# Performance work log

Hardware: AMD Instinct MI355X
Metric: run time of the kernel (lower is better)

## Reference

```python
import jax, jax.numpy as jnp
import numpy as np

N_NODES = 50000
N_EDGES = 800000
D_FEAT = 96
HIDDEN = 96
AVG_DEG = 16.0


def setup_inputs() -> dict:
    key = jax.random.key(0)
    k1, k2, k3, k4, k5 = jax.random.split(key, 5)
    x = jax.random.normal(k1, (N_NODES, D_FEAT), dtype=jnp.float32)
    row = jax.random.randint(k2, (N_EDGES,), 0, N_NODES)
    col = jax.random.randint(k3, (N_EDGES,), 0, N_NODES)
    edge_index = jnp.stack([row, col]).astype(jnp.int32)  # [2, E]
    # normalized adjacency values ~ 1/degree scale
    edge_weight = jax.random.uniform(k4, (N_EDGES,), dtype=jnp.float32) / AVG_DEG
    # init_w: small normal + identity (random=False path)
    W = 0.1 * jax.random.normal(k5, (D_FEAT, HIDDEN), dtype=jnp.float32) + jnp.eye(D_FEAT, HIDDEN, dtype=jnp.float32)
    b = jnp.zeros((HIDDEN,), dtype=jnp.float32)
    return {"x": x, "W": W, "b": b, "edge_index": edge_index, "edge_weight": edge_weight}


def reference(x, W, b, edge_index, edge_weight):
    # dense projection + bias
    h = x @ W + b  # [N, H]
    # sparse adj matmul: out[i] = sum_e w_e * h[col_e] for row_e == i
    row, col = edge_index[0], edge_index[1]
    msgs = edge_weight[:, None] * h[col]  # [E, H]
    pre_nonlinearity = jax.ops.segment_sum(msgs, row, num_segments=N_NODES)  # [N, H]
    # inference path: no dropout (training=None)
    output = jax.nn.elu(pre_nonlinearity)
    return (pre_nonlinearity, output)
```

## Files before the change

kernel.cpp:

```cpp
#include <hip/hip_runtime.h>


#define D 96
#define BSHIFT 5
#define BROWS 32
#define CAP 768
#define CPAD 16
#define EB_CHUNK 3200
#define NBKT_MAX 1600
#define GR 64
#define KP 104

typedef unsigned long long u64;
typedef unsigned short u16;
typedef unsigned int u32;

typedef __attribute__((ext_vector_type(8))) __bf16 bf8_t;
typedef __attribute__((ext_vector_type(8))) short s8_t;
typedef __attribute__((ext_vector_type(4))) float f4_t;

__device__ __forceinline__ u16 f2bf(float f) {
  const u32 u = __float_as_uint(f);
  return (u16)((u + 0x7FFFu + ((u >> 16) & 1u)) >> 16);
}
__device__ __forceinline__ float bf2f(u16 s) {
  return __uint_as_float(((u32)s) << 16);
}

__device__ __forceinline__ f4_t mfma16(s8_t a, s8_t b, f4_t c) {
  return __builtin_amdgcn_mfma_f32_16x16x32_bf16(
      __builtin_bit_cast(bf8_t, a), __builtin_bit_cast(bf8_t, b), c, 0, 0, 0);
}

union __align__(16) FusedSmem {
  struct { u16 hi[96 * KP]; u16 lo[96 * KP]; } w;
  struct { int cnt[NBKT_MAX]; int cur[NBKT_MAX]; int rbuf[EB_CHUNK]; } bz;
};

__global__ __launch_bounds__(256) void fused_gemm_bucketize(
    const float* __restrict__ x, const float* __restrict__ W,
    const float* __restrict__ bias, u16* __restrict__ h16, int n_nodes,
    const int* __restrict__ rows, const int* __restrict__ cols,
    const float* __restrict__ ew, int* __restrict__ bcur,
    u64* __restrict__ tmp, int n_edges, int nbkt, int bb) {
  __shared__ FusedSmem sm;
  const int tid = threadIdx.x;

  if ((int)blockIdx.x < bb) {
    for (int i = tid; i < NBKT_MAX; i += 256) sm.bz.cnt[i] = 0;
    __syncthreads();
    const int e0 = blockIdx.x * EB_CHUNK;
    const int e1 = min(e0 + EB_CHUNK, n_edges);
    for (int e = e0 + tid; e < e1; e += 256) {
      const int r = rows[e];
      sm.bz.rbuf[e - e0] = r;
      atomicAdd(&sm.bz.cnt[r >> BSHIFT], 1);
    }
    __syncthreads();
    for (int b = tid; b < nbkt; b += 256) {
      const int c = sm.bz.cnt[b];
      sm.bz.cur[b] = (c > 0) ? atomicAdd(&bcur[b * CPAD], c) : 0;
    }
    __syncthreads();
    for (int e = e0 + tid; e < e1; e += 256) {
      const int r = sm.bz.rbuf[e - e0];
      const int b = r >> BSHIFT;
      const u64 u = ((u64)__float_as_uint(ew[e]) << 32) |
                    ((u64)(r & (BROWS - 1)) << 20) | (u64)(unsigned)cols[e];
      const int pos = atomicAdd(&sm.bz.cur[b], 1);
      if (pos < CAP) tmp[(size_t)b * CAP + pos] = u;
    }
  } else {
    for (int e = tid; e < 96 * 96; e += 256) {
      const int k = e / 96;
      const int n = e - k * 96;
      const float w = W[e];
      const u16 hb = f2bf(w);
      sm.w.hi[n * KP + k] = hb;
      sm.w.lo[n * KP + k] = f2bf(w - bf2f(hb));
    }
    __syncthreads();

    const int wid = tid >> 6;
    const int lane = tid & 63;
    const int l15 = lane & 15;
    const int g = lane >> 4;
    const int row0 = ((int)blockIdx.x - bb) * GR + wid * 16;

    const int ra = min(row0 + l15, n_nodes - 1);
    const float* xr = x + (size_t)ra * D;
    s8_t ah[3], al[3];
#pragma unroll
    for (int kt = 0; kt < 3; ++kt) {
      const float4 v0 = *(const float4*)(xr + kt * 32 + 8 * g);
      const float4 v1 = *(const float4*)(xr + kt * 32 + 8 * g + 4);
      const float vv[8] = {v0.x, v0.y, v0.z, v0.w, v1.x, v1.y, v1.z, v1.w};
#pragma unroll
      for (int j = 0; j < 8; ++j) {
        const u16 hb = f2bf(vv[j]);
        ah[kt][j] = (short)hb;
        al[kt][j] = (short)f2bf(vv[j] - bf2f(hb));
      }
    }

    f4_t acc[6];
#pragma unroll
    for (int n = 0; n < 6; ++n) {
      const float bv = bias[n * 16 + l15];
      acc[n][0] = bv; acc[n][1] = bv; acc[n][2] = bv; acc[n][3] = bv;
    }

#pragma unroll
    for (int kt = 0; kt < 3; ++kt) {
#pragma unroll
      for (int n = 0; n < 6; ++n) {
        const int wo = (n * 16 + l15) * KP + kt * 32 + 8 * g;
        const s8_t bh = *(const s8_t*)&sm.w.hi[wo];
        const s8_t bl = *(const s8_t*)&sm.w.lo[wo];
        acc[n] = mfma16(ah[kt], bh, acc[n]);
        acc[n] = mfma16(al[kt], bh, acc[n]);
        acc[n] = mfma16(ah[kt], bl, acc[n]);
      }
    }

#pragma unroll
    for (int n = 0; n < 6; ++n) {
#pragma unroll
      for (int r = 0; r < 4; ++r) {
        const int row = row0 + 4 * g + r;
        if (row < n_nodes)
          h16[(size_t)row * D + n * 16 + l15] = f2bf(acc[n][r]);
      }
    }
  }
}

__global__ __launch_bounds__(256) void bucket_gather_kernel(
    const int* __restrict__ bcur, const u64* __restrict__ tmp,
    const u16* __restrict__ h16, float* __restrict__ pre,
    float* __restrict__ out, int n_nodes) {
  __shared__ u64 raw[CAP];
  __shared__ u64 se[CAP];
  __shared__ int cnt[BROWS];
  __shared__ int off[BROWS + 1];
  __shared__ int cur[BROWS];
  const int tid = threadIdx.x;
  const int b = blockIdx.x;
  if (tid < BROWS) cnt[tid] = 0;
  __syncthreads();

  const int base = b * CAP;
  int count = bcur[b * CPAD];
  if (count > CAP) count = CAP;

  for (int k = tid; k < count; k += 256) {
    const u64 u = tmp[base + k];
    raw[k] = u;
    atomicAdd(&cnt[(int)((u >> 20) & (BROWS - 1))], 1);
  }
  __syncthreads();

  if (tid < BROWS) off[tid + 1] = cnt[tid];
  if (tid == 0) off[0] = 0;
  __syncthreads();
  for (int d = 1; d <= BROWS; d <<= 1) {
    int v = 0;
    if (tid <= BROWS && tid >= d) v = off[tid - d];
    __syncthreads();
    if (tid <= BROWS) off[tid] += v;
    __syncthreads();
  }
  if (tid < BROWS) cur[tid] = off[tid];
  __syncthreads();

  for (int k = tid; k < count; k += 256) {
    const u64 u = raw[k];
    const int rl = (int)((u >> 20) & (BROWS - 1));
    se[atomicAdd(&cur[rl], 1)] = u;
  }
  __syncthreads();

  const int g = tid >> 5;
  const int lane = tid & 31;
  const int row0 = b * BROWS;
#pragma unroll
  for (int j = 0; j < 4; ++j) {
    const int r = g * 4 + j;
    const int row = row0 + r;
    const int s = off[r], e = off[r + 1];
    float a0 = 0.f, a1 = 0.f, a2 = 0.f;
    int k = s;
    for (; k + 3 < e; k += 4) {
      const u64 u0 = se[k], u1 = se[k + 1], u2 = se[k + 2], u3 = se[k + 3];
      const u16* h0 = h16 + (size_t)(u0 & 0xFFFFF) * D;
      const u16* h1 = h16 + (size_t)(u1 & 0xFFFFF) * D;
      const u16* h2 = h16 + (size_t)(u2 & 0xFFFFF) * D;
      const u16* h3 = h16 + (size_t)(u3 & 0xFFFFF) * D;
      const float w0 = __uint_as_float((u32)(u0 >> 32));
      const float w1 = __uint_as_float((u32)(u1 >> 32));
      const float w2 = __uint_as_float((u32)(u2 >> 32));
      const float w3 = __uint_as_float((u32)(u3 >> 32));
      const float p00 = bf2f(h0[lane]), p01 = bf2f(h0[lane + 32]), p02 = bf2f(h0[lane + 64]);
      const float p10 = bf2f(h1[lane]), p11 = bf2f(h1[lane + 32]), p12 = bf2f(h1[lane + 64]);
      const float p20 = bf2f(h2[lane]), p21 = bf2f(h2[lane + 32]), p22 = bf2f(h2[lane + 64]);
      const float p30 = bf2f(h3[lane]), p31 = bf2f(h3[lane + 32]), p32 = bf2f(h3[lane + 64]);
      a0 = fmaf(w0, p00, a0); a1 = fmaf(w0, p01, a1); a2 = fmaf(w0, p02, a2);
      a0 = fmaf(w1, p10, a0); a1 = fmaf(w1, p11, a1); a2 = fmaf(w1, p12, a2);
      a0 = fmaf(w2, p20, a0); a1 = fmaf(w2, p21, a1); a2 = fmaf(w2, p22, a2);
      a0 = fmaf(w3, p30, a0); a1 = fmaf(w3, p31, a1); a2 = fmaf(w3, p32, a2);
    }
    for (; k < e; ++k) {
      const u64 u = se[k];
      const u16* hr = h16 + (size_t)(u & 0xFFFFF) * D;
      const float w = __uint_as_float((u32)(u >> 32));
      a0 = fmaf(w, bf2f(hr[lane]), a0);
      a1 = fmaf(w, bf2f(hr[lane + 32]), a1);
      a2 = fmaf(w, bf2f(hr[lane + 64]), a2);
    }
    if (row < n_nodes) {
      float* pr = pre + (size_t)row * D;
      float* orow = out + (size_t)row * D;
      pr[lane] = a0; pr[lane + 32] = a1; pr[lane + 64] = a2;
      orow[lane]      = a0 > 0.f ? a0 : (__expf(a0) - 1.f);
      orow[lane + 32] = a1 > 0.f ? a1 : (__expf(a1) - 1.f);
      orow[lane + 64] = a2 > 0.f ? a2 : (__expf(a2) - 1.f);
    }
  }
}

extern "C" void kernel_launch(void* const* d_in, const int* in_sizes, int n_in,
                              void* d_out, int out_size, void* d_ws, size_t ws_size,
                              hipStream_t stream) {
  const float* x  = (const float*)d_in[0];
  const float* W  = (const float*)d_in[1];
  const float* b  = (const float*)d_in[2];
  const int*   ei = (const int*)d_in[3];
  const float* ew = (const float*)d_in[4];

  const int n_nodes = in_sizes[0] / D;
  const int n_edges = in_sizes[4];
  const int* rows = ei;
  const int* cols = ei + n_edges;

  float* pre  = (float*)d_out;
  float* outp = pre + (size_t)n_nodes * D;

  const int nbkt = (n_nodes + BROWS - 1) / BROWS;

  char* ws = (char*)d_ws;
  u16*  h16  = (u16*)ws;   ws += (size_t)n_nodes * D * sizeof(u16);
  int*  bcur = (int*)ws;   ws += (size_t)nbkt * CPAD * sizeof(int);
  u64*  tmp  = (u64*)ws;

  hipMemsetAsync(bcur, 0, (size_t)nbkt * CPAD * sizeof(int), stream);

  const int gb = (n_nodes + GR - 1) / GR;
  const int bb = (n_edges + EB_CHUNK - 1) / EB_CHUNK;
  fused_gemm_bucketize<<<gb + bb, 256, 0, stream>>>(
      x, W, b, h16, n_nodes, rows, cols, ew, bcur, tmp, n_edges, nbkt, bb);

  bucket_gather_kernel<<<nbkt, 256, 0, stream>>>(bcur, tmp, h16, pre, outp, n_nodes);
}
```

Before: 153.8 us.

## Precompute bf16 hi/lo weight fragments in setup kernel, drop per-block LDS staging

Adds a small setup kernel that zeroes the bucket counters, replacing the memset, and converts W once into MFMA-fragment-ordered bf16 hi/lo arrays in global memory. GEMM blocks now load their B fragments directly from global (L2-resident) memory instead of each block converting W into LDS and synchronizing. The union shared layout shrinks to just the bucketize arrays, and launch bounds ask for 6 blocks per CU to raise occupancy. The cost is an extra kernel launch, and the GEMM path now relies on global or L2 loads for the weights in place of LDS.

```diff
diff --git a/kernel.cpp b/kernel.cpp
--- a/kernel.cpp
+++ b/kernel.cpp
@@ -9,7 +9,7 @@
 #define EB_CHUNK 3200
 #define NBKT_MAX 1600
 #define GR 64
-#define KP 104
+#define NFRAG 18
 
 typedef unsigned long long u64;
 typedef unsigned short u16;
@@ -32,55 +32,68 @@
       __builtin_bit_cast(bf8_t, a), __builtin_bit_cast(bf8_t, b), c, 0, 0, 0);
 }
 
-union __align__(16) FusedSmem {
-  struct { u16 hi[96 * KP]; u16 lo[96 * KP]; } w;
-  struct { int cnt[NBKT_MAX]; int cur[NBKT_MAX]; int rbuf[EB_CHUNK]; } bz;
+__global__ __launch_bounds__(256) void setup_kernel(
+    const float* __restrict__ W, u16* __restrict__ whi, u16* __restrict__ wlo,
+    int* __restrict__ bcur, int nbkt) {
+  const int i = blockIdx.x * 256 + threadIdx.x;
+  if (i < nbkt) bcur[i * CPAD] = 0;
+  if (i < NFRAG * 64) {
+    const int f = i >> 6;
+    const int lane = i & 63;
+    const int n = f / 3, kt = f - 3 * n;
+    const int g = lane >> 4, l15 = lane & 15;
+    const int col = n * 16 + l15;
+#pragma unroll
+    for (int j = 0; j < 8; ++j) {
+      const float w = W[(kt * 32 + 8 * g + j) * D + col];
+      const u16 hb = f2bf(w);
+      whi[(size_t)(f * 64 + lane) * 8 + j] = hb;
+      wlo[(size_t)(f * 64 + lane) * 8 + j] = f2bf(w - bf2f(hb));
+    }
+  }
+}
+
+struct BzSmem {
+  int cnt[NBKT_MAX];
+  int cur[NBKT_MAX];
+  int rbuf[EB_CHUNK];
 };
 
-__global__ __launch_bounds__(256) void fused_gemm_bucketize(
-    const float* __restrict__ x, const float* __restrict__ W,
-    const float* __restrict__ bias, u16* __restrict__ h16, int n_nodes,
+__global__ __launch_bounds__(256, 6) void fused_gemm_bucketize(
+    const float* __restrict__ x, const u16* __restrict__ whi,
+    const u16* __restrict__ wlo, const float* __restrict__ bias,
+    u16* __restrict__ h16, int n_nodes,
     const int* __restrict__ rows, const int* __restrict__ cols,
     const float* __restrict__ ew, int* __restrict__ bcur,
     u64* __restrict__ tmp, int n_edges, int nbkt, int bb) {
-  __shared__ FusedSmem sm;
+  __shared__ BzSmem sm;
   const int tid = threadIdx.x;
 
   if ((int)blockIdx.x < bb) {
-    for (int i = tid; i < NBKT_MAX; i += 256) sm.bz.cnt[i] = 0;
+    for (int i = tid; i < NBKT_MAX; i += 256) sm.cnt[i] = 0;
     __syncthreads();
     const int e0 = blockIdx.x * EB_CHUNK;
     const int e1 = min(e0 + EB_CHUNK, n_edges);
     for (int e = e0 + tid; e < e1; e += 256) {
       const int r = rows[e];
-      sm.bz.rbuf[e - e0] = r;
-      atomicAdd(&sm.bz.cnt[r >> BSHIFT], 1);
+      sm.rbuf[e - e0] = r;
+      atomicAdd(&sm.cnt[r >> BSHIFT], 1);
     }
     __syncthreads();
     for (int b = tid; b < nbkt; b += 256) {
-      const int c = sm.bz.cnt[b];
-      sm.bz.cur[b] = (c > 0) ? atomicAdd(&bcur[b * CPAD], c) : 0;
+      const int c = sm.cnt[b];
+      sm.cur[b] = (c > 0) ? atomicAdd(&bcur[b * CPAD], c) : 0;
     }
     __syncthreads();
     for (int e = e0 + tid; e < e1; e += 256) {
-      const int r = sm.bz.rbuf[e - e0];
+      const int r = sm.rbuf[e - e0];
       const int b = r >> BSHIFT;
       const u64 u = ((u64)__float_as_uint(ew[e]) << 32) |
                     ((u64)(r & (BROWS - 1)) << 20) | (u64)(unsigned)cols[e];
-      const int pos = atomicAdd(&sm.bz.cur[b], 1);
+      const int pos = atomicAdd(&sm.cur[b], 1);
       if (pos < CAP) tmp[(size_t)b * CAP + pos] = u;
     }
   } else {
-    for (int e = tid; e < 96 * 96; e += 256) {
-      const int k = e / 96;
-      const int n = e - k * 96;
-      const float w = W[e];
-      const u16 hb = f2bf(w);
-      sm.w.hi[n * KP + k] = hb;
-      sm.w.lo[n * KP + k] = f2bf(w - bf2f(hb));
-    }
-    __syncthreads();
-
     const int wid = tid >> 6;
     const int lane = tid & 63;
     const int l15 = lane & 15;
@@ -114,9 +127,9 @@
     for (int kt = 0; kt < 3; ++kt) {
 #pragma unroll
       for (int n = 0; n < 6; ++n) {
-        const int wo = (n * 16 + l15) * KP + kt * 32 + 8 * g;
-        const s8_t bh = *(const s8_t*)&sm.w.hi[wo];
-        const s8_t bl = *(const s8_t*)&sm.w.lo[wo];
+        const int f = n * 3 + kt;
+        const s8_t bh = *(const s8_t*)(whi + (size_t)(f * 64 + lane) * 8);
+        const s8_t bl = *(const s8_t*)(wlo + (size_t)(f * 64 + lane) * 8);
         acc[n] = mfma16(ah[kt], bh, acc[n]);
         acc[n] = mfma16(al[kt], bh, acc[n]);
         acc[n] = mfma16(ah[kt], bl, acc[n]);
@@ -250,14 +263,16 @@
   char* ws = (char*)d_ws;
   u16*  h16  = (u16*)ws;   ws += (size_t)n_nodes * D * sizeof(u16);
   int*  bcur = (int*)ws;   ws += (size_t)nbkt * CPAD * sizeof(int);
-  u64*  tmp  = (u64*)ws;
-
-  hipMemsetAsync(bcur, 0, (size_t)nbkt * CPAD * sizeof(int), stream);
+  u64*  tmp  = (u64*)ws;   ws += (size_t)nbkt * CAP * sizeof(u64);
+  u16*  whi  = (u16*)ws;   ws += (size_t)NFRAG * 64 * 8 * sizeof(u16);
+  u16*  wlo  = (u16*)ws;
+
+  setup_kernel<<<(nbkt + 255) / 256, 256, 0, stream>>>(W, whi, wlo, bcur, nbkt);
 
   const int gb = (n_nodes + GR - 1) / GR;
   const int bb = (n_edges + EB_CHUNK - 1) / EB_CHUNK;
   fused_gemm_bucketize<<<gb + bb, 256, 0, stream>>>(
-      x, W, b, h16, n_nodes, rows, cols, ew, bcur, tmp, n_edges, nbkt, bb);
+      x, whi, wlo, b, h16, n_nodes, rows, cols, ew, bcur, tmp, n_edges, nbkt, bb);
 
   bucket_gather_kernel<<<nbkt, 256, 0, stream>>>(bcur, tmp, h16, pre, outp, n_nodes);
 }
```

Result: no change. 151.3 us (-1.7%).
